# Performance work log

Hardware: AMD Instinct MI355X
Metric: run time of the kernel (lower is better)

Reference implementation:

```python
import jax, jax.numpy as jnp
import numpy as np

N_NODES = 50000
N_EDGES = 800000
F_IN = 256
HID = 64
HEADS = 8
N_CLS = 16
NEG_SLOPE = 0.2  # PyG GATConv default


def setup_inputs() -> dict:
    key = jax.random.key(0)
    ks = jax.random.split(key, 10)
    x = jax.random.normal(ks[0], (N_NODES, F_IN), dtype=jnp.float32)
    edge_index = jax.random.randint(ks[1], (2, N_EDGES), 0, N_NODES, dtype=jnp.int32)
    s1 = 1.0 / np.sqrt(F_IN)
    s2 = 1.0 / np.sqrt(HEADS * HID)
    W1 = jax.random.normal(ks[2], (F_IN, HEADS * HID), dtype=jnp.float32) * s1
    att_src1 = jax.random.normal(ks[3], (HEADS, HID), dtype=jnp.float32) * s2
    att_dst1 = jax.random.normal(ks[4], (HEADS, HID), dtype=jnp.float32) * s2
    b1 = jnp.zeros((HEADS * HID,), dtype=jnp.float32)
    W2 = jax.random.normal(ks[5], (HEADS * HID, N_CLS), dtype=jnp.float32) * s2
    att_src2 = jax.random.normal(ks[6], (1, N_CLS), dtype=jnp.float32) * 0.25
    att_dst2 = jax.random.normal(ks[7], (1, N_CLS), dtype=jnp.float32) * 0.25
    b2 = jnp.zeros((N_CLS,), dtype=jnp.float32)
    return {"x": x, "edge_index": edge_index, "W1": W1, "att_src1": att_src1,
            "att_dst1": att_dst1, "b1": b1, "W2": W2, "att_src2": att_src2,
            "att_dst2": att_dst2, "b2": b2}


def gat_conv(x, src, dst, W, a_src, a_dst, b, concat):
    # PyG GATConv (eval mode): h = x W, per-edge score = LeakyReLU(a_src.h_src + a_dst.h_dst),
    # segment softmax over incoming edges of dst, scatter-add aggregation.
    N = x.shape[0]
    H, C = a_src.shape
    h = (x @ W).reshape(N, H, C)                      # [N,H,C]
    e_src = jnp.einsum('nhc,hc->nh', h, a_src)        # [N,H]
    e_dst = jnp.einsum('nhc,hc->nh', h, a_dst)        # [N,H]
    e = jax.nn.leaky_relu(e_src[src] + e_dst[dst], NEG_SLOPE)  # [E,H]
    m = jax.lax.stop_gradient(jax.ops.segment_max(e, dst, num_segments=N))  # [N,H]
    p = jnp.exp(e - m[dst])
    denom = jax.ops.segment_sum(p, dst, num_segments=N)        # [N,H]
    alpha = p / (denom[dst] + 1e-16)                  # [E,H]
    out = jax.ops.segment_sum(alpha[:, :, None] * h[src], dst, num_segments=N)  # [N,H,C]
    out = out.reshape(N, H * C) if concat else out.mean(axis=1)
    return out + b


def reference(x, edge_index, W1, att_src1, att_dst1, b1, W2, att_src2, att_dst2, b2):
    N = x.shape[0]
    loops = jnp.arange(N, dtype=edge_index.dtype)     # add_self_loops=True default
    src = jnp.concatenate([edge_index[0], loops])
    dst = jnp.concatenate([edge_index[1], loops])
    h = gat_conv(x, src, dst, W1, att_src1, att_dst1, b1, concat=True)
    h = jax.nn.elu(h)
    out = gat_conv(h, src, dst, W2, att_src2, att_dst2, b2, concat=False)
    return jax.nn.log_softmax(out, axis=1)
```

## Files before the change

kernel.cpp:

```cpp
#include <hip/hip_runtime.h>
#include <hip/hip_bf16.h>

#define N_NODES 50000
#define N_EDGES 800000
#define E2 (N_EDGES + N_NODES)
#define F_IN 256
#define HID 64
#define HEADS 8
#define HO (HEADS * HID)
#define N_CLS 16
#define NEG_SLOPE 0.2f

typedef short short8 __attribute__((ext_vector_type(8)));
typedef float f32x4 __attribute__((ext_vector_type(4)));

__device__ __forceinline__ float bf2f(unsigned int hi16) { return __uint_as_float(hi16); }
__device__ __forceinline__ unsigned short f2bfu(float f) {
    return __bfloat16_as_ushort(__float2bfloat16(f));
}

__global__ __launch_bounds__(256) void convert_x_kernel(const float4* __restrict__ x,
                                                        uint4* __restrict__ xb) {
    int i = blockIdx.x * blockDim.x + threadIdx.x;
    if (i >= N_NODES * F_IN / 8) return;
    float4 v0 = x[i * 2], v1 = x[i * 2 + 1];
    uint4 o;
    o.x = (unsigned)f2bfu(v0.x) | ((unsigned)f2bfu(v0.y) << 16);
    o.y = (unsigned)f2bfu(v0.z) | ((unsigned)f2bfu(v0.w) << 16);
    o.z = (unsigned)f2bfu(v1.x) | ((unsigned)f2bfu(v1.y) << 16);
    o.w = (unsigned)f2bfu(v1.z) | ((unsigned)f2bfu(v1.w) << 16);
    xb[i] = o;
}

__global__ __launch_bounds__(256) void convert_wt_kernel(const float* __restrict__ W,
                                                         unsigned short* __restrict__ wt) {
    int i = blockIdx.x * blockDim.x + threadIdx.x;
    if (i >= F_IN * HO) return;
    int k = i / HO, n = i % HO;
    wt[n * F_IN + k] = f2bfu(W[i]);
}

__global__ __launch_bounds__(256) void convert_w2_kernel(const float* __restrict__ W2,
                                                         unsigned short* __restrict__ w2p) {
    int idx = blockIdx.x * blockDim.x + threadIdx.x;
    if (idx >= HO * N_CLS) return;
    int j = idx & 7, l = (idx >> 3) & 63, c = idx >> 9;
    int k = c * 32 + ((l >> 4) & 3) * 8 + j;
    int col = l & 15;
    w2p[idx] = f2bfu(W2[k * N_CLS + col]);
}

#define LDK 40
__global__ __launch_bounds__(256) void gemm1_mfma_kernel(const unsigned short* __restrict__ xb,
                                                         const unsigned short* __restrict__ wt,
                                                         const float* __restrict__ as1,
                                                         const float* __restrict__ ad1,
                                                         unsigned short* __restrict__ h1b,
                                                         float* __restrict__ es1,
                                                         float* __restrict__ ed1) {
    __shared__ unsigned short sA[128 * LDK];
    __shared__ unsigned short sB[128 * LDK];
    int t = threadIdx.x;
    int m0 = blockIdx.y * 128, n0 = blockIdx.x * 128;
    int wid = t >> 6, lane = t & 63;
    int wr = wid >> 1, wc = wid & 1;
    int rl = lane & 15, kg = lane >> 4;
    f32x4 zero = {0.f, 0.f, 0.f, 0.f};
    f32x4 acc[4][4];
#pragma unroll
    for (int m = 0; m < 4; m++)
#pragma unroll
        for (int n = 0; n < 4; n++) acc[m][n] = zero;

    int srow = t >> 2, sslot = t & 3;
    for (int k0 = 0; k0 < F_IN; k0 += 32) {
#pragma unroll
        for (int p = 0; p < 2; p++) {
            int r = srow + p * 64;
            int gm = m0 + r;
            uint4 v = {0, 0, 0, 0};
            if (gm < N_NODES) v = *(const uint4*)(xb + (size_t)gm * F_IN + k0 + sslot * 8);
            *(uint4*)(sA + r * LDK + sslot * 8) = v;
        }
#pragma unroll
        for (int p = 0; p < 2; p++) {
            int r = srow + p * 64;
            uint4 v = *(const uint4*)(wt + (size_t)(n0 + r) * F_IN + k0 + sslot * 8);
            *(uint4*)(sB + r * LDK + sslot * 8) = v;
        }
        __syncthreads();
        short8 af[4], bfr[4];
#pragma unroll
        for (int m = 0; m < 4; m++)
            af[m] = *(const short8*)(sA + (wr * 64 + m * 16 + rl) * LDK + kg * 8);
#pragma unroll
        for (int n = 0; n < 4; n++)
            bfr[n] = *(const short8*)(sB + (wc * 64 + n * 16 + rl) * LDK + kg * 8);
#pragma unroll
        for (int m = 0; m < 4; m++)
#pragma unroll
            for (int n = 0; n < 4; n++)
                acc[m][n] = __builtin_amdgcn_mfma_f32_16x16x32_bf16(af[m], bfr[n], acc[m][n], 0, 0, 0);
        __syncthreads();
    }

    int h = (n0 + wc * 64) >> 6;
    float asv[4], adv[4];
#pragma unroll
    for (int n = 0; n < 4; n++) {
        asv[n] = as1[h * HID + n * 16 + rl];
        adv[n] = ad1[h * HID + n * 16 + rl];
    }
#pragma unroll
    for (int m = 0; m < 4; m++) {
#pragma unroll
        for (int reg = 0; reg < 4; reg++) {
            int gr = m0 + wr * 64 + m * 16 + kg * 4 + reg;
            float pa = 0.f, pd = 0.f;
#pragma unroll
            for (int n = 0; n < 4; n++) {
                float v = acc[m][n][reg];
                pa += v * asv[n];
                pd += v * adv[n];
            }
#pragma unroll
            for (int o = 8; o; o >>= 1) { pa += __shfl_xor(pa, o); pd += __shfl_xor(pd, o); }
            if (gr < N_NODES) {
#pragma unroll
                for (int n = 0; n < 4; n++) {
                    int gc = n0 + wc * 64 + n * 16 + rl;
                    h1b[(size_t)gr * HO + gc] = f2bfu(acc[m][n][reg]);
                }
                if (rl == 0) {
                    es1[gr * HEADS + h] = pa;
                    ed1[gr * HEADS + h] = pd;
                }
            }
        }
    }
}

__global__ __launch_bounds__(256) void hist_kernel(const int* __restrict__ ei, int* __restrict__ deg) {
    int e = blockIdx.x * blockDim.x + threadIdx.x;
    if (e >= E2) return;
    int dst = (e < N_EDGES) ? ei[N_EDGES + e] : (e - N_EDGES);
    atomicAdd(&deg[dst], 1);
}

#define NBLK_SCAN ((N_NODES + 255) / 256)
__global__ __launch_bounds__(256) void scan1_kernel(const int* __restrict__ deg, int* __restrict__ bsum) {
    int i = blockIdx.x * 256 + threadIdx.x;
    int v = (i < N_NODES) ? deg[i] : 0;
#pragma unroll
    for (int o = 32; o; o >>= 1) v += __shfl_xor(v, o);
    __shared__ int ws_[4];
    if ((threadIdx.x & 63) == 0) ws_[threadIdx.x >> 6] = v;
    __syncthreads();
    if (threadIdx.x == 0) bsum[blockIdx.x] = ws_[0] + ws_[1] + ws_[2] + ws_[3];
}

__global__ __launch_bounds__(256) void scan2_kernel(const int* __restrict__ bsum, int* __restrict__ bbase) {
    int t = threadIdx.x;
    int v = (t < NBLK_SCAN) ? bsum[t] : 0;
    __shared__ int s[256];
    s[t] = v; __syncthreads();
    for (int o = 1; o < 256; o <<= 1) {
        int tv = (t >= o) ? s[t - o] : 0;
        __syncthreads();
        s[t] += tv;
        __syncthreads();
    }
    if (t < NBLK_SCAN) bbase[t] = s[t] - v;
}

__global__ __launch_bounds__(256) void scan3_kernel(const int* __restrict__ deg,
                                                    const int* __restrict__ bbase,
                                                    int* __restrict__ off) {
    int t = threadIdx.x;
    int i = blockIdx.x * 256 + t;
    int v = (i < N_NODES) ? deg[i] : 0;
    int lane = t & 63, wid = t >> 6;
    int sc = v;
#pragma unroll
    for (int o = 1; o < 64; o <<= 1) {
        int tv = __shfl_up(sc, o);
        if (lane >= o) sc += tv;
    }
    __shared__ int wsum[4];
    if (lane == 63) wsum[wid] = sc;
    __syncthreads();
    int wbase = 0;
    for (int k = 0; k < 4; k++) if (k < wid) wbase += wsum[k];
    if (i < N_NODES) off[i] = bbase[blockIdx.x] + wbase + sc - v;
}

__global__ __launch_bounds__(256) void fill_kernel(const int* __restrict__ ei,
                                                   const int* __restrict__ off,
                                                   int* __restrict__ cursor,
                                                   int* __restrict__ srcs) {
    int e = blockIdx.x * blockDim.x + threadIdx.x;
    if (e >= E2) return;
    int src, dst;
    if (e < N_EDGES) { src = ei[e]; dst = ei[N_EDGES + e]; }
    else { src = dst = e - N_EDGES; }
    int pos = atomicAdd(&cursor[dst], 1);
    srcs[off[dst] + pos] = src;
}

__global__ __launch_bounds__(256) void agg1_kernel(const uint4* __restrict__ h1v,
                                                   const float* __restrict__ es1,
                                                   const float* __restrict__ ed1,
                                                   const int* __restrict__ srcs,
                                                   const int* __restrict__ off,
                                                   const int* __restrict__ deg,
                                                   const float* __restrict__ b1,
                                                   uint4* __restrict__ out1b) {
    int w = (blockIdx.x * blockDim.x + threadIdx.x) >> 6;
    int lane = threadIdx.x & 63;
    if (w >= N_NODES) return;
    int h = lane >> 3;
    int o = off[w], d = deg[w];
    float edv = ed1[w * HEADS + h];
    float den = 0.f;
    float acc[8] = {};
    int s = srcs[o];
    uint4 raw = h1v[(size_t)s * (HO / 8) + lane];
    float esv = es1[s * HEADS + h];
    for (int i = 0; i < d; i++) {
        uint4 raw_n;
        float esv_n;
        if (i + 1 < d) {
            int s2 = srcs[o + i + 1];
            raw_n = h1v[(size_t)s2 * (HO / 8) + lane];
            esv_n = es1[s2 * HEADS + h];
        } else {
            raw_n = raw; esv_n = esv;
        }
        float e = esv + edv;
        e = (e > 0.f) ? e : NEG_SLOPE * e;
        float p = __expf(e);
        den += p;
        acc[0] += p * bf2f(raw.x << 16);
        acc[1] += p * bf2f(raw.x & 0xffff0000u);
        acc[2] += p * bf2f(raw.y << 16);
        acc[3] += p * bf2f(raw.y & 0xffff0000u);
        acc[4] += p * bf2f(raw.z << 16);
        acc[5] += p * bf2f(raw.z & 0xffff0000u);
        acc[6] += p * bf2f(raw.w << 16);
        acc[7] += p * bf2f(raw.w & 0xffff0000u);
        raw = raw_n; esv = esv_n;
    }
    float inv = 1.f / (den + 1e-16f);
    unsigned short s8[8];
#pragma unroll
    for (int k = 0; k < 8; k++) {
        float v = acc[k] * inv + b1[lane * 8 + k];
        v = (v > 0.f) ? v : (__expf(v) - 1.f);
        s8[k] = f2bfu(v);
    }
    uint4 st;
    st.x = (unsigned)s8[0] | ((unsigned)s8[1] << 16);
    st.y = (unsigned)s8[2] | ((unsigned)s8[3] << 16);
    st.z = (unsigned)s8[4] | ((unsigned)s8[5] << 16);
    st.w = (unsigned)s8[6] | ((unsigned)s8[7] << 16);
    out1b[w * (HO / 8) + lane] = st;
}

__global__ __launch_bounds__(256) void layer2_mfma_kernel(const unsigned short* __restrict__ act,
                                                          const unsigned short* __restrict__ w2p,
                                                          const float* __restrict__ as2,
                                                          const float* __restrict__ ad2,
                                                          unsigned short* __restrict__ h2b,
                                                          float* __restrict__ es2,
                                                          float* __restrict__ ed2) {
    int wave = (blockIdx.x * blockDim.x + threadIdx.x) >> 6;
    int lane = threadIdx.x & 63;
    int m0 = wave * 16;
    if (m0 >= N_NODES) return;
    int rl = lane & 15, kg = lane >> 4;
    int row = m0 + rl;
    f32x4 acc = {0.f, 0.f, 0.f, 0.f};
    const unsigned short* arow = act + (size_t)row * HO + kg * 8;
#pragma unroll
    for (int c = 0; c < 16; c++) {
        short8 af = *(const short8*)(arow + c * 32);
        short8 bf = *(const short8*)(w2p + (c * 64 + lane) * 8);
        acc = __builtin_amdgcn_mfma_f32_16x16x32_bf16(af, bf, acc, 0, 0, 0);
    }
    float a_s = as2[rl], a_d = ad2[rl];
#pragma unroll
    for (int reg = 0; reg < 4; reg++) {
        int r = m0 + kg * 4 + reg;
        float v = acc[reg];
        float pa = v * a_s, pd = v * a_d;
#pragma unroll
        for (int o = 8; o; o >>= 1) { pa += __shfl_xor(pa, o); pd += __shfl_xor(pd, o); }
        h2b[r * N_CLS + rl] = f2bfu(v);
        if (rl == 0) { es2[r] = pa; ed2[r] = pd; }
    }
}

__global__ __launch_bounds__(256) void agg2_kernel(const unsigned short* __restrict__ h2b,
                                                   const float* __restrict__ es2,
                                                   const float* __restrict__ ed2,
                                                   const int* __restrict__ srcs,
                                                   const int* __restrict__ off,
                                                   const int* __restrict__ deg,
                                                   const float* __restrict__ b2,
                                                   float* __restrict__ out) {
    int w = (blockIdx.x * blockDim.x + threadIdx.x) >> 6;
    int lane = threadIdx.x & 63;
    if (w >= N_NODES) return;
    int c = lane & 15, j = lane >> 4;
    int o = off[w], d = deg[w];
    float edv = ed2[w];
    float den = 0.f, acc = 0.f;
    for (int i = j; i < d; i += 4) {
        int s = srcs[o + i];
        float e = es2[s] + edv;
        e = (e > 0.f) ? e : NEG_SLOPE * e;
        float p = __expf(e);
        den += p;
        acc += p * bf2f((unsigned)h2b[s * N_CLS + c] << 16);
    }
#pragma unroll
    for (int o2 = 16; o2 <= 32; o2 <<= 1) {
        den += __shfl_xor(den, o2);
        acc += __shfl_xor(acc, o2);
    }
    float v = acc / (den + 1e-16f) + b2[c];
    float mm = v;
#pragma unroll
    for (int o2 = 8; o2; o2 >>= 1) mm = fmaxf(mm, __shfl_xor(mm, o2));
    float se = __expf(v - mm);
#pragma unroll
    for (int o2 = 8; o2; o2 >>= 1) se += __shfl_xor(se, o2);
    if (lane < N_CLS) out[w * N_CLS + c] = v - mm - logf(se);
}

extern "C" void kernel_launch(void* const* d_in, const int* in_sizes, int n_in,
                              void* d_out, int out_size, void* d_ws, size_t ws_size,
                              hipStream_t stream) {
    const float* x   = (const float*)d_in[0];
    const int*   ei  = (const int*)d_in[1];
    const float* W1  = (const float*)d_in[2];
    const float* as1 = (const float*)d_in[3];
    const float* ad1 = (const float*)d_in[4];
    const float* b1  = (const float*)d_in[5];
    const float* W2  = (const float*)d_in[6];
    const float* as2 = (const float*)d_in[7];
    const float* ad2 = (const float*)d_in[8];
    const float* b2  = (const float*)d_in[9];
    float* out = (float*)d_out;

    unsigned short* usw = (unsigned short*)d_ws;
    unsigned short* h1b   = usw;
    unsigned short* xb    = h1b + (size_t)N_NODES * HO;
    unsigned short* wt    = xb + (size_t)N_NODES * F_IN;
    unsigned short* w2p   = wt + F_IN * HO;
    unsigned short* out1b = w2p + HO * N_CLS;
    unsigned short* h2b   = out1b + (size_t)N_NODES * HO;
    float* fw = (float*)(h2b + (size_t)N_NODES * N_CLS);
    float* es1  = fw;
    float* ed1  = es1 + (size_t)N_NODES * HEADS;
    float* es2  = ed1 + (size_t)N_NODES * HEADS;
    float* ed2  = es2 + N_NODES;
    int* deg    = (int*)(ed2 + N_NODES);
    int* cursor = deg + N_NODES;
    int* off    = cursor + N_NODES;
    int* srcs   = off + N_NODES;
    int* bsum   = srcs + E2;
    int* bbase  = bsum + 256;

    hipMemsetAsync(deg, 0, 2 * N_NODES * sizeof(int), stream);

    convert_x_kernel<<<(N_NODES * F_IN / 8 + 255) / 256, 256, 0, stream>>>((const float4*)x, (uint4*)xb);
    convert_wt_kernel<<<(F_IN * HO + 255) / 256, 256, 0, stream>>>(W1, wt);
    convert_w2_kernel<<<(HO * N_CLS + 255) / 256, 256, 0, stream>>>(W2, w2p);

    gemm1_mfma_kernel<<<dim3(HO / 128, (N_NODES + 127) / 128), 256, 0, stream>>>(
        xb, wt, as1, ad1, h1b, es1, ed1);

    hist_kernel<<<(E2 + 255) / 256, 256, 0, stream>>>(ei, deg);
    scan1_kernel<<<NBLK_SCAN, 256, 0, stream>>>(deg, bsum);
    scan2_kernel<<<1, 256, 0, stream>>>(bsum, bbase);
    scan3_kernel<<<NBLK_SCAN, 256, 0, stream>>>(deg, bbase, off);
    fill_kernel<<<(E2 + 255) / 256, 256, 0, stream>>>(ei, off, cursor, srcs);

    agg1_kernel<<<(N_NODES + 3) / 4, 256, 0, stream>>>((const uint4*)h1b, es1, ed1, srcs, off, deg,
                                                       b1, (uint4*)out1b);

    layer2_mfma_kernel<<<((N_NODES / 16) * 64 + 255) / 256, 256, 0, stream>>>(
        out1b, w2p, as2, ad2, h2b, es2, ed2);

    agg2_kernel<<<(N_NODES + 3) / 4, 256, 0, stream>>>(h2b, es2, ed2, srcs, off, deg, b2, out);
}
```

Measured before the change: 420.5 us.

## Slice layer-1 features into 32-column tables and precompute edge attention weights

The GEMM now writes h1 as 16 column slices of 32 features per node, so each aggregation pass gathers from a smaller table that fits in cache. A new per-edge kernel precomputes bf16 exp(leaky_relu) scores for each head in CSR order, using a dst array stored during the fill step. Aggregation is split into 200000 blocks over two phases, with 8 edges processed in parallel per wave and a shuffle reduction at the end. This trades extra passes, extra edge-array traffic and bf16 rounding of the attention weights for better cache locality on the random gathers.

```diff
diff --git a/kernel.cpp b/kernel.cpp
--- a/kernel.cpp
+++ b/kernel.cpp
@@ -4,6 +4,7 @@
 #define N_NODES 50000
 #define N_EDGES 800000
 #define E2 (N_EDGES + N_NODES)
+#define PSTR (E2 + 16)
 #define F_IN 256
 #define HID 64
 #define HEADS 8
@@ -55,7 +56,7 @@
                                                          const unsigned short* __restrict__ wt,
                                                          const float* __restrict__ as1,
                                                          const float* __restrict__ ad1,
-                                                         unsigned short* __restrict__ h1b,
+                                                         unsigned short* __restrict__ h1s,
                                                          float* __restrict__ es1,
                                                          float* __restrict__ ed1) {
     __shared__ unsigned short sA[128 * LDK];
@@ -129,7 +130,9 @@
 #pragma unroll
                 for (int n = 0; n < 4; n++) {
                     int gc = n0 + wc * 64 + n * 16 + rl;
-                    h1b[(size_t)gr * HO + gc] = f2bfu(acc[m][n][reg]);
+                    int slice = gc >> 5;
+                    h1s[(size_t)slice * N_NODES * 32 + (size_t)gr * 32 + (gc & 31)] =
+                        f2bfu(acc[m][n][reg]);
                 }
                 if (rl == 0) {
                     es1[gr * HEADS + h] = pa;
@@ -197,73 +200,101 @@
 __global__ __launch_bounds__(256) void fill_kernel(const int* __restrict__ ei,
                                                    const int* __restrict__ off,
                                                    int* __restrict__ cursor,
-                                                   int* __restrict__ srcs) {
+                                                   int* __restrict__ srcs,
+                                                   int* __restrict__ dsts) {
     int e = blockIdx.x * blockDim.x + threadIdx.x;
     if (e >= E2) return;
     int src, dst;
     if (e < N_EDGES) { src = ei[e]; dst = ei[N_EDGES + e]; }
     else { src = dst = e - N_EDGES; }
     int pos = atomicAdd(&cursor[dst], 1);
-    srcs[off[dst] + pos] = src;
-}
-
-__global__ __launch_bounds__(256) void agg1_kernel(const uint4* __restrict__ h1v,
-                                                   const float* __restrict__ es1,
-                                                   const float* __restrict__ ed1,
+    int slot = off[dst] + pos;
+    srcs[slot] = src;
+    dsts[slot] = dst;
+}
+
+__global__ __launch_bounds__(256) void pk_kernel(const int* __restrict__ srcs,
+                                                 const int* __restrict__ dsts,
+                                                 const float* __restrict__ es1,
+                                                 const float* __restrict__ ed1,
+                                                 unsigned short* __restrict__ pcsr) {
+    int j = blockIdx.x * blockDim.x + threadIdx.x;
+    if (j >= E2) return;
+    int s = srcs[j], d = dsts[j];
+    float4 ea0 = *(const float4*)(es1 + (size_t)s * 8);
+    float4 ea1 = *(const float4*)(es1 + (size_t)s * 8 + 4);
+    float4 eb0 = *(const float4*)(ed1 + (size_t)d * 8);
+    float4 eb1 = *(const float4*)(ed1 + (size_t)d * 8 + 4);
+    float e[8] = {ea0.x + eb0.x, ea0.y + eb0.y, ea0.z + eb0.z, ea0.w + eb0.w,
+                  ea1.x + eb1.x, ea1.y + eb1.y, ea1.z + eb1.z, ea1.w + eb1.w};
+#pragma unroll
+    for (int h = 0; h < 8; h++) {
+        float v = fmaxf(e[h], NEG_SLOPE * e[h]);
+        pcsr[(size_t)h * PSTR + j] = f2bfu(__expf(v));
+    }
+}
+
+__global__ __launch_bounds__(256) void agg1_kernel(const unsigned short* __restrict__ h1s,
+                                                   const unsigned short* __restrict__ pcsr,
                                                    const int* __restrict__ srcs,
                                                    const int* __restrict__ off,
                                                    const int* __restrict__ deg,
                                                    const float* __restrict__ b1,
-                                                   uint4* __restrict__ out1b) {
-    int w = (blockIdx.x * blockDim.x + threadIdx.x) >> 6;
-    int lane = threadIdx.x & 63;
-    if (w >= N_NODES) return;
-    int h = lane >> 3;
-    int o = off[w], d = deg[w];
-    float edv = ed1[w * HEADS + h];
-    float den = 0.f;
-    float acc[8] = {};
-    int s = srcs[o];
-    uint4 raw = h1v[(size_t)s * (HO / 8) + lane];
-    float esv = es1[s * HEADS + h];
-    for (int i = 0; i < d; i++) {
-        uint4 raw_n;
-        float esv_n;
-        if (i + 1 < d) {
-            int s2 = srcs[o + i + 1];
-            raw_n = h1v[(size_t)s2 * (HO / 8) + lane];
-            esv_n = es1[s2 * HEADS + h];
-        } else {
-            raw_n = raw; esv_n = esv;
-        }
-        float e = esv + edv;
-        e = (e > 0.f) ? e : NEG_SLOPE * e;
-        float p = __expf(e);
+                                                   unsigned short* __restrict__ out1b) {
+    int b = blockIdx.x;
+    int phase = b / 100000;
+    int r = b - phase * 100000;
+    int slice = phase * 8 + (r & 7);
+    int wid = threadIdx.x >> 6, lane = threadIdx.x & 63;
+    int node = (r >> 3) * 4 + wid;
+    int head = slice >> 1;
+    int sub = lane >> 3;
+    int fl = lane & 7;
+    int o = off[node], d = deg[node];
+    const unsigned short* tab = h1s + (size_t)slice * N_NODES * 32;
+    const unsigned short* ph = pcsr + (size_t)head * PSTR;
+    float den = 0.f, acc0 = 0.f, acc1 = 0.f, acc2 = 0.f, acc3 = 0.f;
+    int iters = (d + 7) >> 3;
+    for (int it = 0; it < iters; ++it) {
+        int idx = it * 8 + sub;
+        int slot = o + idx;
+        bool valid = idx < d;
+        unsigned short pb = __builtin_nontemporal_load(ph + slot);
+        int s = __builtin_nontemporal_load(srcs + slot);
+        float p = bf2f((unsigned)pb << 16);
+        p = valid ? p : 0.f;
+        s = valid ? s : 0;
+        uint2 raw = *(const uint2*)(tab + (size_t)s * 32 + fl * 4);
         den += p;
-        acc[0] += p * bf2f(raw.x << 16);
-        acc[1] += p * bf2f(raw.x & 0xffff0000u);
-        acc[2] += p * bf2f(raw.y << 16);
-        acc[3] += p * bf2f(raw.y & 0xffff0000u);
-        acc[4] += p * bf2f(raw.z << 16);
-        acc[5] += p * bf2f(raw.z & 0xffff0000u);
-        acc[6] += p * bf2f(raw.w << 16);
-        acc[7] += p * bf2f(raw.w & 0xffff0000u);
-        raw = raw_n; esv = esv_n;
-    }
-    float inv = 1.f / (den + 1e-16f);
-    unsigned short s8[8];
-#pragma unroll
-    for (int k = 0; k < 8; k++) {
-        float v = acc[k] * inv + b1[lane * 8 + k];
-        v = (v > 0.f) ? v : (__expf(v) - 1.f);
-        s8[k] = f2bfu(v);
-    }
-    uint4 st;
-    st.x = (unsigned)s8[0] | ((unsigned)s8[1] << 16);
-    st.y = (unsigned)s8[2] | ((unsigned)s8[3] << 16);
-    st.z = (unsigned)s8[4] | ((unsigned)s8[5] << 16);
-    st.w = (unsigned)s8[6] | ((unsigned)s8[7] << 16);
-    out1b[w * (HO / 8) + lane] = st;
+        acc0 += p * bf2f(raw.x << 16);
+        acc1 += p * bf2f(raw.x & 0xffff0000u);
+        acc2 += p * bf2f(raw.y << 16);
+        acc3 += p * bf2f(raw.y & 0xffff0000u);
+    }
+#pragma unroll
+    for (int m = 8; m <= 32; m <<= 1) {
+        den  += __shfl_xor(den, m);
+        acc0 += __shfl_xor(acc0, m);
+        acc1 += __shfl_xor(acc1, m);
+        acc2 += __shfl_xor(acc2, m);
+        acc3 += __shfl_xor(acc3, m);
+    }
+    if (lane < 8) {
+        float inv = 1.f / (den + 1e-16f);
+        int fb = slice * 32 + fl * 4;
+        float v0 = acc0 * inv + b1[fb + 0];
+        float v1 = acc1 * inv + b1[fb + 1];
+        float v2 = acc2 * inv + b1[fb + 2];
+        float v3 = acc3 * inv + b1[fb + 3];
+        v0 = (v0 > 0.f) ? v0 : (__expf(v0) - 1.f);
+        v1 = (v1 > 0.f) ? v1 : (__expf(v1) - 1.f);
+        v2 = (v2 > 0.f) ? v2 : (__expf(v2) - 1.f);
+        v3 = (v3 > 0.f) ? v3 : (__expf(v3) - 1.f);
+        unsigned lo = (unsigned)f2bfu(v0) | ((unsigned)f2bfu(v1) << 16);
+        unsigned hi = (unsigned)f2bfu(v2) | ((unsigned)f2bfu(v3) << 16);
+        unsigned long long pk64 = (unsigned long long)lo | ((unsigned long long)hi << 32);
+        __builtin_nontemporal_store(pk64, (unsigned long long*)(out1b + (size_t)node * HO + fb));
+    }
 }
 
 __global__ __launch_bounds__(256) void layer2_mfma_kernel(const unsigned short* __restrict__ act,
@@ -354,13 +385,14 @@
     float* out = (float*)d_out;
 
     unsigned short* usw = (unsigned short*)d_ws;
-    unsigned short* h1b   = usw;
-    unsigned short* xb    = h1b + (size_t)N_NODES * HO;
+    unsigned short* h1s   = usw;
+    unsigned short* xb    = h1s + (size_t)N_NODES * HO;
     unsigned short* wt    = xb + (size_t)N_NODES * F_IN;
     unsigned short* w2p   = wt + F_IN * HO;
     unsigned short* out1b = w2p + HO * N_CLS;
     unsigned short* h2b   = out1b + (size_t)N_NODES * HO;
-    float* fw = (float*)(h2b + (size_t)N_NODES * N_CLS);
+    unsigned short* pcsr  = h2b + (size_t)N_NODES * N_CLS;
+    float* fw = (float*)(pcsr + (size_t)HEADS * PSTR);
     float* es1  = fw;
     float* ed1  = es1 + (size_t)N_NODES * HEADS;
     float* es2  = ed1 + (size_t)N_NODES * HEADS;
@@ -369,7 +401,8 @@
     int* cursor = deg + N_NODES;
     int* off    = cursor + N_NODES;
     int* srcs   = off + N_NODES;
-    int* bsum   = srcs + E2;
+    int* dsts   = srcs + PSTR;
+    int* bsum   = dsts + E2;
     int* bbase  = bsum + 256;
 
     hipMemsetAsync(deg, 0, 2 * N_NODES * sizeof(int), stream);
@@ -379,16 +412,17 @@
     convert_w2_kernel<<<(HO * N_CLS + 255) / 256, 256, 0, stream>>>(W2, w2p);
 
     gemm1_mfma_kernel<<<dim3(HO / 128, (N_NODES + 127) / 128), 256, 0, stream>>>(
-        xb, wt, as1, ad1, h1b, es1, ed1);
+        xb, wt, as1, ad1, h1s, es1, ed1);
 
     hist_kernel<<<(E2 + 255) / 256, 256, 0, stream>>>(ei, deg);
     scan1_kernel<<<NBLK_SCAN, 256, 0, stream>>>(deg, bsum);
     scan2_kernel<<<1, 256, 0, stream>>>(bsum, bbase);
     scan3_kernel<<<NBLK_SCAN, 256, 0, stream>>>(deg, bbase, off);
-    fill_kernel<<<(E2 + 255) / 256, 256, 0, stream>>>(ei, off, cursor, srcs);
-
-    agg1_kernel<<<(N_NODES + 3) / 4, 256, 0, stream>>>((const uint4*)h1b, es1, ed1, srcs, off, deg,
-                                                       b1, (uint4*)out1b);
+    fill_kernel<<<(E2 + 255) / 256, 256, 0, stream>>>(ei, off, cursor, srcs, dsts);
+
+    pk_kernel<<<(E2 + 255) / 256, 256, 0, stream>>>(srcs, dsts, es1, ed1, pcsr);
+
+    agg1_kernel<<<200000, 256, 0, stream>>>(h1s, pcsr, srcs, off, deg, b1, out1b);
 
     layer2_mfma_kernel<<<((N_NODES / 16) * 64 + 255) / 256, 256, 0, stream>>>(
         out1b, w2p, as2, ad2, h2b, es2, ed2);
```

After: 692.1 us. 1.65x slower.

## Fuse x bf16 conversion into GEMM1 and layer-2 projection into agg1

Applied to the files above, without the earlier changes.

The standalone x-to-bf16 conversion kernel is removed; GEMM1 now loads fp32 x and packs it to bf16 while filling shared memory. The layer-2 projection (W2 matmul plus attention dot products) moves into the agg1 kernel. Each block builds a transposed bf16 W2 in LDS, stages each node's ELU output row in LDS and computes the 16-class projection with scalar FMAs, so the out1b intermediate (N x 512 bf16) is never written or re-read. The cost is a W2 rebuild in every agg1 block, extra LDS use that may lower occupancy, and scalar FMAs in place of MFMA. The grid is also assumed to divide the node count evenly.

```diff
diff --git a/kernel.cpp b/kernel.cpp
--- a/kernel.cpp
+++ b/kernel.cpp
@@ -18,18 +18,8 @@
 __device__ __forceinline__ unsigned short f2bfu(float f) {
     return __bfloat16_as_ushort(__float2bfloat16(f));
 }
-
-__global__ __launch_bounds__(256) void convert_x_kernel(const float4* __restrict__ x,
-                                                        uint4* __restrict__ xb) {
-    int i = blockIdx.x * blockDim.x + threadIdx.x;
-    if (i >= N_NODES * F_IN / 8) return;
-    float4 v0 = x[i * 2], v1 = x[i * 2 + 1];
-    uint4 o;
-    o.x = (unsigned)f2bfu(v0.x) | ((unsigned)f2bfu(v0.y) << 16);
-    o.y = (unsigned)f2bfu(v0.z) | ((unsigned)f2bfu(v0.w) << 16);
-    o.z = (unsigned)f2bfu(v1.x) | ((unsigned)f2bfu(v1.y) << 16);
-    o.w = (unsigned)f2bfu(v1.z) | ((unsigned)f2bfu(v1.w) << 16);
-    xb[i] = o;
+__device__ __forceinline__ unsigned packbf(float a, float b) {
+    return (unsigned)f2bfu(a) | ((unsigned)f2bfu(b) << 16);
 }
 
 __global__ __launch_bounds__(256) void convert_wt_kernel(const float* __restrict__ W,
@@ -40,18 +30,8 @@
     wt[n * F_IN + k] = f2bfu(W[i]);
 }
 
-__global__ __launch_bounds__(256) void convert_w2_kernel(const float* __restrict__ W2,
-                                                         unsigned short* __restrict__ w2p) {
-    int idx = blockIdx.x * blockDim.x + threadIdx.x;
-    if (idx >= HO * N_CLS) return;
-    int j = idx & 7, l = (idx >> 3) & 63, c = idx >> 9;
-    int k = c * 32 + ((l >> 4) & 3) * 8 + j;
-    int col = l & 15;
-    w2p[idx] = f2bfu(W2[k * N_CLS + col]);
-}
-
 #define LDK 40
-__global__ __launch_bounds__(256) void gemm1_mfma_kernel(const unsigned short* __restrict__ xb,
+__global__ __launch_bounds__(256) void gemm1_mfma_kernel(const float* __restrict__ x,
                                                          const unsigned short* __restrict__ wt,
                                                          const float* __restrict__ as1,
                                                          const float* __restrict__ ad1,
@@ -79,7 +59,15 @@
             int r = srow + p * 64;
             int gm = m0 + r;
             uint4 v = {0, 0, 0, 0};
-            if (gm < N_NODES) v = *(const uint4*)(xb + (size_t)gm * F_IN + k0 + sslot * 8);
+            if (gm < N_NODES) {
+                const float* xg = x + (size_t)gm * F_IN + k0 + sslot * 8;
+                float4 a0 = *(const float4*)xg;
+                float4 a1 = *(const float4*)(xg + 4);
+                v.x = packbf(a0.x, a0.y);
+                v.y = packbf(a0.z, a0.w);
+                v.z = packbf(a1.x, a1.y);
+                v.w = packbf(a1.z, a1.w);
+            }
             *(uint4*)(sA + r * LDK + sslot * 8) = v;
         }
 #pragma unroll
@@ -214,10 +202,23 @@
                                                    const int* __restrict__ off,
                                                    const int* __restrict__ deg,
                                                    const float* __restrict__ b1,
-                                                   uint4* __restrict__ out1b) {
-    int w = (blockIdx.x * blockDim.x + threadIdx.x) >> 6;
-    int lane = threadIdx.x & 63;
-    if (w >= N_NODES) return;
+                                                   const float* __restrict__ W2,
+                                                   const float* __restrict__ as2,
+                                                   const float* __restrict__ ad2,
+                                                   unsigned short* __restrict__ h2b,
+                                                   float* __restrict__ es2,
+                                                   float* __restrict__ ed2) {
+    __shared__ unsigned w2t[16 * 257];
+    __shared__ unsigned rowbuf[4][256];
+    int t = threadIdx.x;
+    for (int i = t; i < 16 * 256; i += 256) {
+        int cls = i >> 8, k = i & 255;
+        w2t[cls * 257 + k] = packbf(W2[(2 * k) * N_CLS + cls], W2[(2 * k + 1) * N_CLS + cls]);
+    }
+    __syncthreads();
+
+    int wid = t >> 6, lane = t & 63;
+    int w = blockIdx.x * 4 + wid;
     int h = lane >> 3;
     int o = off[w], d = deg[w];
     float edv = ed1[w * HEADS + h];
@@ -251,53 +252,33 @@
         raw = raw_n; esv = esv_n;
     }
     float inv = 1.f / (den + 1e-16f);
-    unsigned short s8[8];
+    float r[8];
 #pragma unroll
     for (int k = 0; k < 8; k++) {
         float v = acc[k] * inv + b1[lane * 8 + k];
-        v = (v > 0.f) ? v : (__expf(v) - 1.f);
-        s8[k] = f2bfu(v);
-    }
-    uint4 st;
-    st.x = (unsigned)s8[0] | ((unsigned)s8[1] << 16);
-    st.y = (unsigned)s8[2] | ((unsigned)s8[3] << 16);
-    st.z = (unsigned)s8[4] | ((unsigned)s8[5] << 16);
-    st.w = (unsigned)s8[6] | ((unsigned)s8[7] << 16);
-    out1b[w * (HO / 8) + lane] = st;
-}
-
-__global__ __launch_bounds__(256) void layer2_mfma_kernel(const unsigned short* __restrict__ act,
-                                                          const unsigned short* __restrict__ w2p,
-                                                          const float* __restrict__ as2,
-                                                          const float* __restrict__ ad2,
-                                                          unsigned short* __restrict__ h2b,
-                                                          float* __restrict__ es2,
-                                                          float* __restrict__ ed2) {
-    int wave = (blockIdx.x * blockDim.x + threadIdx.x) >> 6;
-    int lane = threadIdx.x & 63;
-    int m0 = wave * 16;
-    if (m0 >= N_NODES) return;
-    int rl = lane & 15, kg = lane >> 4;
-    int row = m0 + rl;
-    f32x4 acc = {0.f, 0.f, 0.f, 0.f};
-    const unsigned short* arow = act + (size_t)row * HO + kg * 8;
-#pragma unroll
-    for (int c = 0; c < 16; c++) {
-        short8 af = *(const short8*)(arow + c * 32);
-        short8 bf = *(const short8*)(w2p + (c * 64 + lane) * 8);
-        acc = __builtin_amdgcn_mfma_f32_16x16x32_bf16(af, bf, acc, 0, 0, 0);
-    }
-    float a_s = as2[rl], a_d = ad2[rl];
-#pragma unroll
-    for (int reg = 0; reg < 4; reg++) {
-        int r = m0 + kg * 4 + reg;
-        float v = acc[reg];
-        float pa = v * a_s, pd = v * a_d;
-#pragma unroll
-        for (int o = 8; o; o >>= 1) { pa += __shfl_xor(pa, o); pd += __shfl_xor(pd, o); }
-        h2b[r * N_CLS + rl] = f2bfu(v);
-        if (rl == 0) { es2[r] = pa; ed2[r] = pd; }
-    }
+        r[k] = (v > 0.f) ? v : (__expf(v) - 1.f);
+    }
+#pragma unroll
+    for (int k = 0; k < 4; k++)
+        rowbuf[wid][lane * 4 + k] = packbf(r[2 * k], r[2 * k + 1]);
+    __syncthreads();
+
+    int cls = lane & 15, q = lane >> 4;
+    const unsigned* wrow = &w2t[cls * 257 + q * 64];
+    const unsigned* rrow = &rowbuf[wid][q * 64];
+    float hacc = 0.f;
+#pragma unroll 8
+    for (int kk = 0; kk < 64; kk++) {
+        unsigned rv = rrow[kk], wv = wrow[kk];
+        hacc += bf2f(rv << 16) * bf2f(wv << 16) + bf2f(rv & 0xffff0000u) * bf2f(wv & 0xffff0000u);
+    }
+    hacc += __shfl_xor(hacc, 16);
+    hacc += __shfl_xor(hacc, 32);
+    float sa = hacc * as2[cls], sd = hacc * ad2[cls];
+#pragma unroll
+    for (int o2 = 8; o2; o2 >>= 1) { sa += __shfl_xor(sa, o2); sd += __shfl_xor(sd, o2); }
+    if (lane < N_CLS) h2b[(size_t)w * N_CLS + cls] = f2bfu(hacc);
+    if (lane == 0) { es2[w] = sa; ed2[w] = sd; }
 }
 
 __global__ __launch_bounds__(256) void agg2_kernel(const unsigned short* __restrict__ h2b,
@@ -354,12 +335,9 @@
     float* out = (float*)d_out;
 
     unsigned short* usw = (unsigned short*)d_ws;
-    unsigned short* h1b   = usw;
-    unsigned short* xb    = h1b + (size_t)N_NODES * HO;
-    unsigned short* wt    = xb + (size_t)N_NODES * F_IN;
-    unsigned short* w2p   = wt + F_IN * HO;
-    unsigned short* out1b = w2p + HO * N_CLS;
-    unsigned short* h2b   = out1b + (size_t)N_NODES * HO;
+    unsigned short* h1b  = usw;
+    unsigned short* wt   = h1b + (size_t)N_NODES * HO;
+    unsigned short* h2b  = wt + F_IN * HO;
     float* fw = (float*)(h2b + (size_t)N_NODES * N_CLS);
     float* es1  = fw;
     float* ed1  = es1 + (size_t)N_NODES * HEADS;
@@ -369,17 +347,15 @@
     int* cursor = deg + N_NODES;
     int* off    = cursor + N_NODES;
     int* srcs   = off + N_NODES;
-    int* bsum   = srcs + E2;
+    int* bsum   = srcs + E2 + 16;
     int* bbase  = bsum + 256;
 
     hipMemsetAsync(deg, 0, 2 * N_NODES * sizeof(int), stream);
 
-    convert_x_kernel<<<(N_NODES * F_IN / 8 + 255) / 256, 256, 0, stream>>>((const float4*)x, (uint4*)xb);
     convert_wt_kernel<<<(F_IN * HO + 255) / 256, 256, 0, stream>>>(W1, wt);
-    convert_w2_kernel<<<(HO * N_CLS + 255) / 256, 256, 0, stream>>>(W2, w2p);
 
     gemm1_mfma_kernel<<<dim3(HO / 128, (N_NODES + 127) / 128), 256, 0, stream>>>(
-        xb, wt, as1, ad1, h1b, es1, ed1);
+        x, wt, as1, ad1, h1b, es1, ed1);
 
     hist_kernel<<<(E2 + 255) / 256, 256, 0, stream>>>(ei, deg);
     scan1_kernel<<<NBLK_SCAN, 256, 0, stream>>>(deg, bsum);
@@ -387,11 +363,8 @@
     scan3_kernel<<<NBLK_SCAN, 256, 0, stream>>>(deg, bbase, off);
     fill_kernel<<<(E2 + 255) / 256, 256, 0, stream>>>(ei, off, cursor, srcs);
 
-    agg1_kernel<<<(N_NODES + 3) / 4, 256, 0, stream>>>((const uint4*)h1b, es1, ed1, srcs, off, deg,
-                                                       b1, (uint4*)out1b);
-
-    layer2_mfma_kernel<<<((N_NODES / 16) * 64 + 255) / 256, 256, 0, stream>>>(
-        out1b, w2p, as2, ad2, h2b, es2, ed2);
+    agg1_kernel<<<N_NODES / 4, 256, 0, stream>>>((const uint4*)h1b, es1, ed1, srcs, off, deg,
+                                                 b1, W2, as2, ad2, h2b, es2, ed2);
 
     agg2_kernel<<<(N_NODES + 3) / 4, 256, 0, stream>>>(h2b, es2, ed2, srcs, off, deg, b2, out);
 }
```

New measurement: 487.7 us. 16.0% more time.
